# Optimization experiments

Hardware: AMD Instinct MI355X
Metric: run time of the kernel (lower is better)

Reference implementation:

```python
import jax, jax.numpy as jnp
import numpy as np

N, D, F, C = 50000, 32, 128, 16
LN_EPS = 1e-5
CLAMP_MIN = 1e-5


def _layernorm_1d(x):
    # LayerNorm over the full node vector, no affine (elementwise_affine=False)
    m = x.mean()
    v = x.var()  # biased, matches torch LayerNorm
    return (x - m) / jnp.sqrt(v + LN_EPS)


def setup_inputs() -> dict:
    key = jax.random.key(0)
    k1, k2, k3, k4, k5, k6 = jax.random.split(key, 6)
    return {
        "h": jax.random.normal(k1, (N, F), dtype=jnp.float32),
        "logits": jax.random.normal(k2, (N, C), dtype=jnp.float32),
        "old_z": jax.random.uniform(k3, (N,), dtype=jnp.float32),
        "tau_1": jax.random.uniform(k4, (1,), dtype=jnp.float32),
        "tau_2": jax.random.uniform(k5, (1,), dtype=jnp.float32),
        "nbr": jax.random.randint(k6, (N, D), 0, N, dtype=jnp.int32),
    }


def reference(h, logits, old_z, tau_1, tau_2, nbr):
    # --- mailbox pass 1: neighbor logits -> adaptive gating features ---
    pred = jnp.argmax(logits[nbr], axis=2)          # [N, D] neighbor class preds
    center_pred = jnp.argmax(logits, axis=1)        # [N]
    # n_degree = 1 in the source (counts, not fractions) -- reproduced faithfully
    f1 = jnp.sum(pred == center_pred[:, None], axis=1).astype(h.dtype)  # [N]
    cnts = jax.nn.one_hot(pred, C, dtype=h.dtype).sum(axis=1)           # [N, C]
    cnts_p = jnp.clip(cnts, CLAMP_MIN, None)
    f2 = -jnp.sum(cnts_p * jnp.log(cnts_p), axis=1)                     # [N]
    f1 = jax.lax.stop_gradient(f1)
    f2 = jax.lax.stop_gradient(f2)

    norm_f1 = _layernorm_1d(f1)
    norm_f2 = _layernorm_1d(f2)
    # shared_tau=True path: tau_1, tau_2 passed in ([1] broadcasts over [N])
    z = jax.nn.sigmoid(-(norm_f1 - tau_1)) * jax.nn.sigmoid(-(norm_f2 - tau_2))  # [N]
    gate = jnp.minimum(old_z, z)

    # --- mailbox pass 2: scatter-sum of neighbor features ---
    agg = h[nbr].sum(axis=1)                        # [N, F]
    normagg = jax.nn.relu(agg)
    new_h = h + gate[:, None] * normagg
    return new_h, z
```

## Files before the change

kernel.cpp:

```cpp
#include <hip/hip_runtime.h>
#include <math.h>

#define NN 50000
#define DEG 32
#define FDIM 128
#define NCLS 16
#define LN_EPS 1e-5f
#define CLAMP_MIN 1e-5f

#define PRED_NB 196
#define CONV_NB 512
#define NGROUPS (NN * FDIM / 8)
#define FEAT_NB 196

typedef float  nf4 __attribute__((ext_vector_type(4)));
typedef unsigned nu4 __attribute__((ext_vector_type(4)));

__device__ inline unsigned bf_rne(float x) {
    unsigned u = __float_as_uint(x);
    u += 0x7fffu + ((u >> 16) & 1u);
    return u >> 16;
}

__global__ __launch_bounds__(256) void k_pre(const float* __restrict__ logits,
                                             unsigned char* __restrict__ pred8,
                                             const float* __restrict__ h,
                                             unsigned* __restrict__ hb) {
    int b = blockIdx.x;
    if (b < PRED_NB) {
        int i = b * 256 + threadIdx.x;
        if (i >= NN) return;
        const nf4* lp = (const nf4*)(logits + (long)i * NCLS);
        float best = -INFINITY;
        int bi = 0;
#pragma unroll
        for (int q = 0; q < 4; ++q) {
            nf4 v = __builtin_nontemporal_load(lp + q);
#pragma unroll
            for (int r = 0; r < 4; ++r) {
                if (v[r] > best) { best = v[r]; bi = q * 4 + r; }
            }
        }
        pred8[i] = (unsigned char)bi;
    } else {
        int g0 = (b - PRED_NB) * 256 + threadIdx.x;
        for (int g = g0; g < NGROUPS; g += CONV_NB * 256) {
            const nf4* src = (const nf4*)(h + (long)g * 8);
            nf4 a = __builtin_nontemporal_load(src);
            nf4 c = __builtin_nontemporal_load(src + 1);
            nu4 o;
            o.x = bf_rne(a.x) | (bf_rne(a.y) << 16);
            o.y = bf_rne(a.z) | (bf_rne(a.w) << 16);
            o.z = bf_rne(c.x) | (bf_rne(c.y) << 16);
            o.w = bf_rne(c.z) | (bf_rne(c.w) << 16);
            ((nu4*)hb)[g] = o;
        }
    }
}

__global__ __launch_bounds__(256) void k_feats_lds(const int* __restrict__ nbr,
                                                   const unsigned char* __restrict__ pred8,
                                                   float* __restrict__ f1,
                                                   float* __restrict__ f2,
                                                   float* __restrict__ partials, int n) {
    __shared__ unsigned char lp[NN];
    {
        const uint4* s4 = (const uint4*)pred8;
        uint4* d4 = (uint4*)lp;
        for (int i = threadIdx.x; i < 3125; i += 256) d4[i] = s4[i];
    }
    __syncthreads();
    int node = blockIdx.x * 256 + threadIdx.x;
    float v1 = 0.f, v2 = 0.f;
    if (node < n) {
        unsigned long long lo = 0ull, hi = 0ull;
        const int4* np = (const int4*)(nbr + (long)node * DEG);
#pragma unroll
        for (int q = 0; q < 8; ++q) {
            int4 k4 = np[q];
            int ks[4] = {k4.x, k4.y, k4.z, k4.w};
#pragma unroll
            for (int r = 0; r < 4; ++r) {
                int p = lp[ks[r]];
                unsigned long long inc = 1ull << ((p & 7) * 8);
                if (p < 8) lo += inc; else hi += inc;
            }
        }
        int cp = lp[node];
        unsigned long long src = (cp < 8) ? lo : hi;
        v1 = (float)((src >> ((cp & 7) * 8)) & 0xffull);
        float ent = 0.f;
#pragma unroll
        for (int c = 0; c < NCLS; ++c) {
            unsigned long long s = (c < 8) ? lo : hi;
            float cnt = (float)((s >> ((c & 7) * 8)) & 0xffull);
            float x = fmaxf(cnt, CLAMP_MIN);
            ent -= x * logf(x);
        }
        v2 = ent;
        f1[node] = v1;
        f2[node] = v2;
    }
    float s0 = v1, s1 = v1 * v1, s2 = v2, s3 = v2 * v2;
#pragma unroll
    for (int off = 32; off > 0; off >>= 1) {
        s0 += __shfl_down(s0, off);
        s1 += __shfl_down(s1, off);
        s2 += __shfl_down(s2, off);
        s3 += __shfl_down(s3, off);
    }
    __shared__ float red[4][4];
    int wid = threadIdx.x >> 6;
    if ((threadIdx.x & 63) == 0) {
        red[wid][0] = s0; red[wid][1] = s1; red[wid][2] = s2; red[wid][3] = s3;
    }
    __syncthreads();
    if (threadIdx.x == 0) {
        float t0 = 0.f, t1 = 0.f, t2 = 0.f, t3 = 0.f;
#pragma unroll
        for (int w = 0; w < 4; ++w) {
            t0 += red[w][0]; t1 += red[w][1]; t2 += red[w][2]; t3 += red[w][3];
        }
        float* pp = partials + (long)blockIdx.x * 4;
        pp[0] = t0; pp[1] = t1; pp[2] = t2; pp[3] = t3;
    }
}

__global__ __launch_bounds__(256) void k_params(const float* __restrict__ partials,
                                                int nb, float* __restrict__ params) {
    double s0 = 0, s1 = 0, s2 = 0, s3 = 0;
    for (int b = threadIdx.x; b < nb; b += 256) {
        const float* pp = partials + (long)b * 4;
        s0 += (double)pp[0]; s1 += (double)pp[1];
        s2 += (double)pp[2]; s3 += (double)pp[3];
    }
#pragma unroll
    for (int off = 32; off > 0; off >>= 1) {
        s0 += __shfl_down(s0, off);
        s1 += __shfl_down(s1, off);
        s2 += __shfl_down(s2, off);
        s3 += __shfl_down(s3, off);
    }
    __shared__ double red[4][4];
    int wid = threadIdx.x >> 6;
    if ((threadIdx.x & 63) == 0) {
        red[wid][0] = s0; red[wid][1] = s1; red[wid][2] = s2; red[wid][3] = s3;
    }
    __syncthreads();
    if (threadIdx.x == 0) {
        double t0 = 0, t1 = 0, t2 = 0, t3 = 0;
        for (int w = 0; w < 4; ++w) {
            t0 += red[w][0]; t1 += red[w][1]; t2 += red[w][2]; t3 += red[w][3];
        }
        double inv_n = 1.0 / (double)NN;
        double m1 = t0 * inv_n;
        double var1 = t1 * inv_n - m1 * m1;
        double m2 = t2 * inv_n;
        double var2 = t3 * inv_n - m2 * m2;
        params[0] = (float)m1;
        params[1] = (float)(1.0 / sqrt(var1 + (double)LN_EPS));
        params[2] = (float)m2;
        params[3] = (float)(1.0 / sqrt(var2 + (double)LN_EPS));
    }
}

__global__ __launch_bounds__(256) void k_agg_bf(const unsigned* __restrict__ hb,
                                                const int* __restrict__ nbr,
                                                const float* __restrict__ old_z,
                                                const float* __restrict__ tau1,
                                                const float* __restrict__ tau2,
                                                const float* __restrict__ f1,
                                                const float* __restrict__ f2,
                                                const float* __restrict__ params,
                                                float* __restrict__ out_h,
                                                float* __restrict__ out_z, int n) {
    int t = blockIdx.x * 256 + threadIdx.x;
    int node = t >> 5;
    int lane = threadIdx.x & 31;
    if (node >= n) return;
    int k = __builtin_nontemporal_load(nbr + (long)node * DEG + lane);
    float4 acc = make_float4(0.f, 0.f, 0.f, 0.f);
#pragma unroll
    for (int jj = 0; jj < 4; ++jj) {
        uint2 vs[8];
#pragma unroll
        for (int j = 0; j < 8; ++j) {
            int kj = __shfl(k, jj * 8 + j, 32);
            vs[j] = ((const uint2*)(hb + (long)kj * (FDIM / 2)))[lane];
        }
#pragma unroll
        for (int j = 0; j < 8; ++j) {
            acc.x += __uint_as_float(vs[j].x << 16);
            acc.y += __uint_as_float(vs[j].x & 0xffff0000u);
            acc.z += __uint_as_float(vs[j].y << 16);
            acc.w += __uint_as_float(vs[j].y & 0xffff0000u);
        }
    }
    float a = (f1[node] - params[0]) * params[1] - tau1[0];
    float b = (f2[node] - params[2]) * params[3] - tau2[0];
    float z = 1.f / ((1.f + expf(a)) * (1.f + expf(b)));
    float gate = fminf(old_z[node], z);
    uint2 hid = ((const uint2*)(hb + (long)node * (FDIM / 2)))[lane];
    nf4 o;
    o.x = __uint_as_float(hid.x << 16)         + gate * fmaxf(acc.x, 0.f);
    o.y = __uint_as_float(hid.x & 0xffff0000u) + gate * fmaxf(acc.y, 0.f);
    o.z = __uint_as_float(hid.y << 16)         + gate * fmaxf(acc.z, 0.f);
    o.w = __uint_as_float(hid.y & 0xffff0000u) + gate * fmaxf(acc.w, 0.f);
    __builtin_nontemporal_store(o, (nf4*)(out_h + (long)node * FDIM) + lane);
    if (lane == 0) __builtin_nontemporal_store(z, out_z + node);
}

extern "C" void kernel_launch(void* const* d_in, const int* in_sizes, int n_in,
                              void* d_out, int out_size, void* d_ws, size_t ws_size,
                              hipStream_t stream) {
    const float* h      = (const float*)d_in[0];
    const float* logits = (const float*)d_in[1];
    const float* old_z  = (const float*)d_in[2];
    const float* tau1   = (const float*)d_in[3];
    const float* tau2   = (const float*)d_in[4];
    const int*   nbr    = (const int*)d_in[5];

    char* ws = (char*)d_ws;
    float*         params   = (float*)ws;
    float*         partials = (float*)(ws + 64);
    unsigned char* pred8    = (unsigned char*)(ws + 32768);
    float*         f1       = (float*)(ws + 90112);
    float*         f2       = (float*)(ws + 294912);
    unsigned*      hb       = (unsigned*)(ws + 524288);

    float* out_h = (float*)d_out;
    float* out_z = out_h + (long)NN * FDIM;

    k_pre     <<<PRED_NB + CONV_NB, 256, 0, stream>>>(logits, pred8, h, hb);
    k_feats_lds<<<FEAT_NB, 256, 0, stream>>>(nbr, pred8, f1, f2, partials, NN);
    k_params  <<<1, 256, 0, stream>>>(partials, FEAT_NB, params);
    k_agg_bf  <<<(NN * DEG + 255) / 256, 256, 0, stream>>>(hb, nbr, old_z, tau1, tau2,
                                                           f1, f2, params, out_h, out_z, NN);
}
```

Before: 145.6 us.

## Split bf16 feature table into four column slabs for cache-local gathers

The bf16 copy of h is stored as four 32-column slabs instead of row-major. The aggregation kernel now runs one grid segment per slab, with 8 lanes per node. Each gather therefore touches a 3.2MB slab that can stay resident in L2/MALL rather than spanning the full 12.8MB table. The cost is that neighbor indices, gate math and f1/f2 reads are repeated once per slab, and each gather is now a 64-byte row segment.

```diff
diff --git a/kernel.cpp b/kernel.cpp
--- a/kernel.cpp
+++ b/kernel.cpp
@@ -13,8 +13,14 @@
 #define NGROUPS (NN * FDIM / 8)
 #define FEAT_NB 196
 
+#define SLICES 4
+#define SL_U32 (NN * 16)
+#define AGG_BPS ((NN * 8 + 255) / 256)
+#define AGG_NB (SLICES * AGG_BPS)
+
 typedef float  nf4 __attribute__((ext_vector_type(4)));
 typedef unsigned nu4 __attribute__((ext_vector_type(4)));
+typedef int    ni4 __attribute__((ext_vector_type(4)));
 
 __device__ inline unsigned bf_rne(float x) {
     unsigned u = __float_as_uint(x);
@@ -53,7 +59,10 @@
             o.y = bf_rne(a.z) | (bf_rne(a.w) << 16);
             o.z = bf_rne(c.x) | (bf_rne(c.y) << 16);
             o.w = bf_rne(c.z) | (bf_rne(c.w) << 16);
-            ((nu4*)hb)[g] = o;
+            int node = g >> 4;
+            int q    = (g >> 2) & 3;
+            int sub  = g & 3;
+            ((nu4*)hb)[(size_t)q * (NN * 4) + node * 4 + sub] = o;
         }
     }
 }
@@ -164,7 +173,7 @@
     }
 }
 
-__global__ __launch_bounds__(256) void k_agg_bf(const unsigned* __restrict__ hb,
+__global__ __launch_bounds__(256) void k_agg_sl(const unsigned* __restrict__ hb,
                                                 const int* __restrict__ nbr,
                                                 const float* __restrict__ old_z,
                                                 const float* __restrict__ tau1,
@@ -174,40 +183,43 @@
                                                 const float* __restrict__ params,
                                                 float* __restrict__ out_h,
                                                 float* __restrict__ out_z, int n) {
-    int t = blockIdx.x * 256 + threadIdx.x;
-    int node = t >> 5;
-    int lane = threadIdx.x & 31;
+    int q = blockIdx.x / AGG_BPS;
+    int t = (blockIdx.x - q * AGG_BPS) * 256 + threadIdx.x;
+    int node = t >> 3;
+    int lane = t & 7;
     if (node >= n) return;
-    int k = __builtin_nontemporal_load(nbr + (long)node * DEG + lane);
+    const unsigned* slab = hb + (size_t)q * SL_U32;
+    ni4 k4 = __builtin_nontemporal_load((const ni4*)(nbr + (long)node * DEG) + lane);
+    int ks[4] = {k4.x, k4.y, k4.z, k4.w};
     float4 acc = make_float4(0.f, 0.f, 0.f, 0.f);
 #pragma unroll
-    for (int jj = 0; jj < 4; ++jj) {
+    for (int c = 0; c < 4; ++c) {
         uint2 vs[8];
 #pragma unroll
-        for (int j = 0; j < 8; ++j) {
-            int kj = __shfl(k, jj * 8 + j, 32);
-            vs[j] = ((const uint2*)(hb + (long)kj * (FDIM / 2)))[lane];
-        }
-#pragma unroll
-        for (int j = 0; j < 8; ++j) {
-            acc.x += __uint_as_float(vs[j].x << 16);
-            acc.y += __uint_as_float(vs[j].x & 0xffff0000u);
-            acc.z += __uint_as_float(vs[j].y << 16);
-            acc.w += __uint_as_float(vs[j].y & 0xffff0000u);
+        for (int s = 0; s < 8; ++s) {
+            int kj = __shfl(ks[c], s, 8);
+            vs[s] = ((const uint2*)(slab + (size_t)kj * 16))[lane];
+        }
+#pragma unroll
+        for (int s = 0; s < 8; ++s) {
+            acc.x += __uint_as_float(vs[s].x << 16);
+            acc.y += __uint_as_float(vs[s].x & 0xffff0000u);
+            acc.z += __uint_as_float(vs[s].y << 16);
+            acc.w += __uint_as_float(vs[s].y & 0xffff0000u);
         }
     }
     float a = (f1[node] - params[0]) * params[1] - tau1[0];
     float b = (f2[node] - params[2]) * params[3] - tau2[0];
     float z = 1.f / ((1.f + expf(a)) * (1.f + expf(b)));
     float gate = fminf(old_z[node], z);
-    uint2 hid = ((const uint2*)(hb + (long)node * (FDIM / 2)))[lane];
+    uint2 hid = ((const uint2*)(slab + (size_t)node * 16))[lane];
     nf4 o;
     o.x = __uint_as_float(hid.x << 16)         + gate * fmaxf(acc.x, 0.f);
     o.y = __uint_as_float(hid.x & 0xffff0000u) + gate * fmaxf(acc.y, 0.f);
     o.z = __uint_as_float(hid.y << 16)         + gate * fmaxf(acc.z, 0.f);
     o.w = __uint_as_float(hid.y & 0xffff0000u) + gate * fmaxf(acc.w, 0.f);
-    __builtin_nontemporal_store(o, (nf4*)(out_h + (long)node * FDIM) + lane);
-    if (lane == 0) __builtin_nontemporal_store(z, out_z + node);
+    __builtin_nontemporal_store(o, (nf4*)(out_h + (long)node * FDIM + q * 32) + lane);
+    if (q == 0 && lane == 0) __builtin_nontemporal_store(z, out_z + node);
 }
 
 extern "C" void kernel_launch(void* const* d_in, const int* in_sizes, int n_in,
@@ -231,9 +243,9 @@
     float* out_h = (float*)d_out;
     float* out_z = out_h + (long)NN * FDIM;
 
-    k_pre     <<<PRED_NB + CONV_NB, 256, 0, stream>>>(logits, pred8, h, hb);
+    k_pre      <<<PRED_NB + CONV_NB, 256, 0, stream>>>(logits, pred8, h, hb);
     k_feats_lds<<<FEAT_NB, 256, 0, stream>>>(nbr, pred8, f1, f2, partials, NN);
-    k_params  <<<1, 256, 0, stream>>>(partials, FEAT_NB, params);
-    k_agg_bf  <<<(NN * DEG + 255) / 256, 256, 0, stream>>>(hb, nbr, old_z, tau1, tau2,
-                                                           f1, f2, params, out_h, out_z, NN);
-}
+    k_params   <<<1, 256, 0, stream>>>(partials, FEAT_NB, params);
+    k_agg_sl   <<<AGG_NB, 256, 0, stream>>>(hb, nbr, old_z, tau1, tau2,
+                                            f1, f2, params, out_h, out_z, NN);
+}
```

Measured after the change: 146.4 us. No clear change (+0.6%).
